# Kernel tuning notes

Hardware: AMD Instinct MI355X
Metric: run time of the kernel (lower is better)

Reference implementation:

```python
import jax, jax.numpy as jnp
import numpy as np

D_FEAT = 8192   # feature-space dimension d
T_RES = 2048    # number of reservoir feature vectors
P_PARAMS = 16   # n_modes * ansatz_layers
ORDER = 16      # agp_krylov_order (Krylov/Lanczos subspace size)
DTAU = 0.08     # cfg.ite_dtau
REG = 1e-4      # cfg.agp_reg
EPS = 1e-15


def setup_inputs() -> dict:
    key = jax.random.key(0)
    k1, k2, k3 = jax.random.split(key, 3)
    f = jax.random.normal(k1, (D_FEAT,), jnp.float32)
    # scale so spectral radius of H = -R^T R times DTAU is O(1)
    R = jax.random.normal(k2, (T_RES, D_FEAT), jnp.float32) * 0.02
    D = jax.random.normal(k3, (P_PARAMS, D_FEAT), jnp.float32)
    return {"f": f, "R": R, "D": D}


def _forward(f, R, D):
    d = f.shape[0]
    l = ORDER

    def apply_H(v):
        # H v = -sum_t f_t (f_t . v)  == -R^T (R v), matrix-free, memory-bound
        return -jnp.einsum('td,t->d', R, jnp.einsum('td,d->t', R, v))

    # ITE residual F = -(H - E) f, E = <f, Hf> / <f, f>
    Hf = apply_H(f)
    E = jnp.dot(f, Hf) / (jnp.dot(f, f) + EPS)
    F = -(Hf - E * f)
    normF = jnp.linalg.norm(F)

    # Lanczos with full reorthogonalisation; Q has l+1 rows (last is scratch)
    Q0 = jnp.zeros((l + 1, d), f.dtype).at[0].set(F / normF)
    alpha0 = jnp.zeros((l,), f.dtype)
    beta0 = jnp.zeros((l,), f.dtype)

    def step(carry, j):
        Q, alpha, beta = carry
        qj = Q[j]
        w = apply_H(qj)
        a = jnp.dot(qj, w)
        alpha = alpha.at[j].set(a)
        w = w - a * qj
        jm1 = jnp.maximum(j - 1, 0)
        bprev = jnp.where(j > 0, beta[jm1], jnp.array(0.0, f.dtype))
        w = w - bprev * Q[jm1]
        # full reorthogonalisation; rows > j of Q are zero so this projects
        # exactly onto span{q_0..q_j} like the original k-loop
        w = w - jnp.einsum('kd,k->d', Q, jnp.einsum('kd,d->k', Q, w))
        b = jnp.linalg.norm(w)
        beta = beta.at[j].set(b)
        Q = Q.at[j + 1].set(w / jnp.maximum(b, 1e-30))
        return (Q, alpha, beta), None

    (Q, alpha, beta), _ = jax.lax.scan(step, (Q0, alpha0, beta0), jnp.arange(l))
    Qb = Q[:l]          # (l, d) orthonormal Krylov basis
    off = beta[:l - 1]  # off-diagonal of tridiagonal T

    # Krylov exponential: exp(-H dtau) F ~= ||F|| * Q^T expm(-T dtau) e0
    Tmat = jnp.diag(alpha) + jnp.diag(off, 1) + jnp.diag(off, -1)
    evals, V = jnp.linalg.eigh(Tmat)
    coeffs = normF * (V @ (jnp.exp(-evals * DTAU) * V[0]))
    direction = jnp.einsum('l,ld->d', coeffs, Qb)

    # per-parameter diagonal projection: dtheta_i = <df_i, dir>/(||df_i||^2 + reg)
    dtheta = (D @ direction) / (jnp.sum(D * D, axis=1) + REG)
    return dtheta


def reference(f, R, D):
    return _forward(f, R, D)
```

## Files before the change

### kernel.cpp

```cpp
#include <hip/hip_runtime.h>
#include <math.h>

#define D_FEAT 8192
#define NC4    2048
#define T_RES  2048
#define LORD   16

#define NTHR 512
#define NBLK 256
#define RPT  32
#define NBAR 40
#define LPAD 16

#define G_COEF  0
#define G_BARC  16
#define G_RELW  (G_BARC + NBAR*64*LPAD)
#define G_ZEND  (G_RELW + NBAR*64*LPAD)
#define G_URAW  G_ZEND
#define G_UUP   (G_URAW + 17*2048)
#define G_FFP   (G_UUP + 256)
#define G_B2P   (G_FFP + 256)
#define G_DP    (G_B2P + 16*256)
#define G_NUMP  (G_DP + 16*17*256)
#define G_DENP  (G_NUMP + 16*256)
#define G_UPB   ((G_DENP + 16*256 + 1023) & ~1023)

__device__ __forceinline__ void astore(float* p, float v) {
    __hip_atomic_store(p, v, __ATOMIC_RELAXED, __HIP_MEMORY_SCOPE_AGENT);
}
__device__ __forceinline__ unsigned aloadu(const unsigned* p) {
    return __hip_atomic_load(p, __ATOMIC_RELAXED, __HIP_MEMORY_SCOPE_AGENT);
}

__device__ __forceinline__ void gbar(unsigned* cnt, unsigned* rel,
                                     int idx, int bid) {
    __syncthreads();
    const int tid = threadIdx.x;
    if (tid == 0)
        __hip_atomic_fetch_add(&cnt[(idx*64 + (bid & 63))*LPAD], 1u,
                               __ATOMIC_RELAXED, __HIP_MEMORY_SCOPE_AGENT);
    if (bid == 0) {
        if (tid < 64) {
            while (aloadu(&cnt[(idx*64 + tid)*LPAD]) < 4u)
                __builtin_amdgcn_s_sleep(1);
            __hip_atomic_store(&rel[(idx*64 + tid)*LPAD], 1u,
                               __ATOMIC_RELAXED, __HIP_MEMORY_SCOPE_AGENT);
        }
    } else if (tid == 0) {
        while (aloadu(&rel[(idx*64 + (bid & 63))*LPAD]) == 0u)
            __builtin_amdgcn_s_sleep(1);
    }
    __syncthreads();
}

__device__ __forceinline__ float wave_sum64(float s) {
    #pragma unroll
    for (int m = 1; m < 64; m <<= 1) s += __shfl_xor(s, m, 64);
    return s;
}

__device__ __forceinline__ void u_pass_lds(const float4 (&rr)[RPT],
                                           const float* wsl, float* ubuf,
                                           int rg, int cg) {
    const float4 w4 = ((const float4*)wsl)[cg];
    #pragma unroll
    for (int i = 0; i < RPT; ++i) {
        float d = rr[i].x*w4.x + rr[i].y*w4.y + rr[i].z*w4.z + rr[i].w*w4.w;
        d += __shfl_xor(d, 1, 64);
        d += __shfl_xor(d, 2, 64);
        d += __shfl_xor(d, 4, 64);
        if (cg == 0) ubuf[rg + 64*i] = d;
    }
}

__device__ __forceinline__ void flush_up(float* UP, const float* ubuf,
                                         int bid, int tid) {
    #pragma unroll
    for (int r = 0; r < 4; ++r) {
        const int t = tid + 512*r;
        astore(&UP[(size_t)(t >> 3)*2048 + bid*8 + (tid & 7)], ubuf[t]);
    }
}

__device__ __forceinline__ void reduce_up(const float* __restrict__ UP,
                                          float* udst, float (*red2)[8],
                                          float* ufin, float* uhrow,
                                          int bid, int tid) {
    const int off = tid & 7, g = tid >> 3;
    const float* base = UP + (size_t)bid*2048;
    float s = 0.f;
    #pragma unroll
    for (int i = 0; i < 4; ++i) s += base[(4*g + i)*8 + off];
    red2[g][off] = s;
    __syncthreads();
    if (tid < 8) {
        float u = 0.f;
        #pragma unroll
        for (int g2 = 0; g2 < 64; ++g2) u += red2[g2][tid];
        ufin[tid] = u;
        uhrow[tid] = u;
        astore(&udst[8*bid + tid], u);
    }
    __syncthreads();
}

__device__ __forceinline__ float4 y_pass(const float4 (&rr)[RPT],
                                         const float* u, int rg) {
    float4 acc = make_float4(0.f, 0.f, 0.f, 0.f);
    #pragma unroll
    for (int i = 0; i < RPT; ++i) {
        const float ut = u[rg + 64*i];
        acc.x -= ut*rr[i].x; acc.y -= ut*rr[i].y;
        acc.z -= ut*rr[i].z; acc.w -= ut*rr[i].w;
    }
    return acc;
}

__device__ __forceinline__ void y_reduce(float4 acc, float (*red)[8][4],
                                         float* ysl, int wave, int lane, int tid) {
    #pragma unroll
    for (int m = 8; m < 64; m <<= 1) {
        acc.x += __shfl_xor(acc.x, m, 64); acc.y += __shfl_xor(acc.y, m, 64);
        acc.z += __shfl_xor(acc.z, m, 64); acc.w += __shfl_xor(acc.w, m, 64);
    }
    if (lane < 8) {
        red[wave][lane][0] = acc.x; red[wave][lane][1] = acc.y;
        red[wave][lane][2] = acc.z; red[wave][lane][3] = acc.w;
    }
    __syncthreads();
    if (tid < 32) {
        const int g = tid >> 2, comp = tid & 3;
        float s = 0.f;
        #pragma unroll
        for (int w = 0; w < 8; ++w) s += red[w][g][comp];
        ysl[g*4 + comp] = s;
    }
    __syncthreads();
}

__global__ __launch_bounds__(NTHR, 2) void k_all(
    const float* __restrict__ Rm, const float* __restrict__ f,
    const float* __restrict__ Dm, float* __restrict__ out,
    float* __restrict__ ws)
{
    __shared__ __align__(16) float ubuf[2048];
    __shared__ float red2[64][8];
    __shared__ float red[8][8][4];
    __shared__ float ufin[8];
    __shared__ float uh[17][8];
    __shared__ __align__(16) float ysl[32];
    __shared__ __align__(16) float dirs[32];
    __shared__ __align__(16) float fsl[32];
    __shared__ float Wh[LORD][32];
    __shared__ float bh[LORD];
    __shared__ float alph[LORD];
    __shared__ float dotl[LORD];
    __shared__ float cf[LORD];
    __shared__ float misc[4];

    float* coefg   = ws + G_COEF;
    unsigned* barc = (unsigned*)(ws + G_BARC);
    unsigned* relw = (unsigned*)(ws + G_RELW);
    float* uraw = ws + G_URAW;
    float* UUP  = ws + G_UUP;
    float* FFP  = ws + G_FFP;
    float* B2P  = ws + G_B2P;
    float* DP   = ws + G_DP;
    float* NUMP = ws + G_NUMP;
    float* DENP = ws + G_DENP;
    float* UPB  = ws + G_UPB;
    int bar = 0;

    const int tid = threadIdx.x, bid = blockIdx.x;
    const int cg = tid & 7, rg = tid >> 3;
    const int lane = tid & 63, wave = tid >> 6;

    const float4* R4 = (const float4*)Rm;
    float4 rr[RPT];
    #pragma unroll
    for (int i = 0; i < RPT; ++i)
        rr[i] = R4[(size_t)(rg + 64*i)*NC4 + (bid << 3) + cg];

    if (wave == 0) {
        float4 fv = make_float4(0.f, 0.f, 0.f, 0.f);
        if (lane < 8) { fv = ((const float4*)f)[(bid << 3) + lane];
                        ((float4*)fsl)[lane] = fv; }
        float s2 = fv.x*fv.x + fv.y*fv.y + fv.z*fv.z + fv.w*fv.w;
        s2 += __shfl_xor(s2, 1, 64);
        s2 += __shfl_xor(s2, 2, 64);
        s2 += __shfl_xor(s2, 4, 64);
        if (lane == 0) astore(&FFP[bid], s2);
    }
    __syncthreads();
    u_pass_lds(rr, fsl, ubuf, rg, cg);
    __syncthreads();
    flush_up(UPB + (size_t)16*NBLK*2048, ubuf, bid, tid);
    gbar(barc, relw, bar++, bid);

    reduce_up(UPB + (size_t)16*NBLK*2048, uraw + 16*2048, red2, ufin, uh[16],
              bid, tid);
    if (tid == 0) {
        float pd = 0.f;
        #pragma unroll
        for (int t = 0; t < 8; ++t) pd += ufin[t]*ufin[t];
        astore(&UUP[bid], pd);
    }
    if (wave == 1) {
        float s = 0.f;
        #pragma unroll
        for (int i = 0; i < 4; ++i) s += FFP[lane + 64*i];
        s = wave_sum64(s);
        if (lane == 0) misc[2] = s;
    }
    gbar(barc, relw, bar++, bid);

    if (wave == 0) {
        float s = 0.f;
        #pragma unroll
        for (int i = 0; i < 4; ++i) s += UUP[lane + 64*i];
        s = wave_sum64(s);
        if (lane == 0) misc[3] = s;
    }
    #pragma unroll
    for (int r = 0; r < 4; ++r)
        ubuf[tid + 512*r] = uraw[16*2048 + tid + 512*r];
    __syncthreads();
    {
        float4 acc = y_pass(rr, ubuf, rg);
        y_reduce(acc, red, ysl, wave, lane, tid);
        const float E = -misc[3] / (misc[2] + 1e-15f);
        float v = 0.f;
        if (tid < 32) { v = E*fsl[tid] - ysl[tid]; Wh[0][tid] = v; }
        if (wave == 0) {
            float s = (lane < 32) ? v*v : 0.f;
            s = wave_sum64(s);
            if (lane == 0) astore(&B2P[0*256 + bid], s);
        }
        __syncthreads();
        u_pass_lds(rr, Wh[0], ubuf, rg, cg);
        __syncthreads();
        flush_up(UPB + (size_t)0*NBLK*2048, ubuf, bid, tid);
    }
    gbar(barc, relw, bar++, bid);

    for (int j = 0; j < LORD; ++j) {
        float* UPj = UPB + (size_t)j*NBLK*2048;
        float* DPj = DP + (size_t)j*17*256;
        reduce_up(UPj, uraw + (size_t)j*2048, red2, ufin, uh[j], bid, tid);
        if (wave == 0 && lane <= j) {
            float pd = 0.f;
            #pragma unroll 1
            for (int t = 0; t < 8; ++t) pd += ufin[t] * uh[lane][t];
            astore(&DPj[lane*256 + bid], pd);
        }
        if (wave == 1) {
            float s = 0.f;
            #pragma unroll
            for (int i = 0; i < 4; ++i) s += B2P[j*256 + lane + 64*i];
            s = wave_sum64(s);
            if (lane == 0) misc[0] = s;
        }
        gbar(barc, relw, bar++, bid);

        float tmp[4];
        if (j < LORD - 1) {
            #pragma unroll
            for (int r = 0; r < 4; ++r)
                tmp[r] = uraw[(size_t)j*2048 + tid + 512*r];
        }
        for (int k = wave; k <= j; k += 8) {
            float s = 0.f;
            #pragma unroll
            for (int i = 0; i < 4; ++i) s += DPj[k*256 + lane + 64*i];
            s = wave_sum64(s);
            if (lane == 0) dotl[k] = s;
        }
        __syncthreads();
        const float b2j = misc[0];
        const float bj  = sqrtf(fmaxf(b2j, 1e-60f));
        if (tid == 0) {
            bh[j]   = bj;
            alph[j] = -dotl[j] / fmaxf(b2j, 1e-60f);
        }
        if (j < LORD - 1) {
            const float inv = 1.0f / bj;
            #pragma unroll
            for (int r = 0; r < 4; ++r) ubuf[tid + 512*r] = tmp[r] * inv;
            __syncthreads();
            float4 acc = y_pass(rr, ubuf, rg);
            y_reduce(acc, red, ysl, wave, lane, tid);
            float v = 0.f;
            if (tid < 32) {
                v = ysl[tid];
                for (int k = 0; k <= j; ++k)
                    v += (dotl[k] / (bj * bh[k] * bh[k])) * Wh[k][tid];
                Wh[j+1][tid] = v;
            }
            if (wave == 0) {
                float s = (lane < 32) ? v*v : 0.f;
                s = wave_sum64(s);
                if (lane == 0) astore(&B2P[(j+1)*256 + bid], s);
            }
            __syncthreads();
            u_pass_lds(rr, Wh[j+1], ubuf, rg, cg);
            __syncthreads();
            flush_up(UPB + (size_t)(j+1)*NBLK*2048, ubuf, bid, tid);
        } else {
            __syncthreads();
            if (bid == 0 && wave == 0) {
                double a = 0.0, bl = 0.0;
                if (lane < LORD)     a  = (double)alph[lane];
                if (lane < LORD - 1) bl = (double)bh[lane + 1];
                double bprev = __shfl_up(bl, 1, 64);
                if (lane == 0) bprev = 0.0;
                if (lane >= LORD) { a = 0.0; bl = 0.0; bprev = 0.0; }
                double v = (lane == 0) ? 1.0 : 0.0;
                double accd = v;
                for (int n = 1; n <= 30; ++n) {
                    double vm = __shfl_up(v, 1, 64);
                    if (lane == 0) vm = 0.0;
                    double vp = __shfl_down(v, 1, 64);
                    if (lane >= LORD - 1) vp = 0.0;
                    const double tv = a*v + bprev*vm + bl*vp;
                    v = tv * (-0.08 / (double)n);
                    accd += v;
                }
                if (lane < LORD)
                    astore(&coefg[lane], (float)accd * bh[0]);
            }
        }
        gbar(barc, relw, bar++, bid);
    }

    if (wave == 0 && lane < 16) cf[lane] = coefg[lane];
    __syncthreads();
    if (tid < 32) {
        float s = 0.f;
        #pragma unroll
        for (int l = 0; l < LORD; ++l) s += cf[l] * Wh[l][tid] / bh[l];
        dirs[tid] = s;
    }
    __syncthreads();
    if (wave == 0 && lane < 16) {
        const float4* Dp = (const float4*)Dm + (size_t)lane*NC4 + (bid << 3);
        float num = 0.f, den = 0.f;
        #pragma unroll
        for (int g = 0; g < 8; ++g) {
            const float4 dv = Dp[g];
            const float4 dr = ((const float4*)dirs)[g];
            num += dv.x*dr.x + dv.y*dr.y + dv.z*dr.z + dv.w*dr.w;
            den += dv.x*dv.x + dv.y*dv.y + dv.z*dv.z + dv.w*dv.w;
        }
        astore(&NUMP[lane*256 + bid], num);
        astore(&DENP[lane*256 + bid], den);
    }
    gbar(barc, relw, bar++, bid);

    if (bid == 0) {
        for (int p = wave; p < 16; p += 8) {
            float n = 0.f, d = 0.f;
            #pragma unroll
            for (int i = 0; i < 4; ++i) {
                n += NUMP[p*256 + lane + 64*i];
                d += DENP[p*256 + lane + 64*i];
            }
            n = wave_sum64(n);
            d = wave_sum64(d);
            if (lane == 0) out[p] = n / (d + 1e-4f);
        }
    }
}

extern "C" void kernel_launch(void* const* d_in, const int* in_sizes, int n_in,
                              void* d_out, int out_size, void* d_ws, size_t ws_size,
                              hipStream_t stream)
{
    (void)in_sizes; (void)n_in; (void)out_size; (void)ws_size;
    const float* f  = (const float*)d_in[0];
    const float* Rm = (const float*)d_in[1];
    const float* Dm = (const float*)d_in[2];
    float* outp = (float*)d_out;
    float* ws   = (float*)d_ws;
    hipMemsetAsync(ws, 0, G_ZEND * sizeof(float), stream);
    void* args[] = { (void*)&Rm, (void*)&f, (void*)&Dm, (void*)&outp, (void*)&ws };
    hipLaunchCooperativeKernel((const void*)k_all, dim3(NBLK), dim3(NTHR),
                               args, 0, stream);
}
```

Baseline: 310.5 us.

## Replace centralized grid barrier with per-block flags and all-poll waits

Replaces the counter/release grid barrier, where block 0 gathers arrivals and then releases everyone, with per-block flag arrays. Each block sets its flag and 64 lanes poll all 256 flags directly, which removes the serial gather-then-release round trip. The partial u-pass results are now written straight to global memory instead of staging through LDS, and only block 0 waits at the final barrier. In exchange every block polls 256 flags at each barrier, adding memory traffic, and the flags depend on the workspace being zeroed before each launch.

New measurement: 383.7 us. +23.6%, slower.

```diff
diff --git a/kernel.cpp b/kernel.cpp
--- a/kernel.cpp
+++ b/kernel.cpp
@@ -9,13 +9,13 @@
 #define NTHR 512
 #define NBLK 256
 #define RPT  32
-#define NBAR 40
-#define LPAD 16
 
 #define G_COEF  0
-#define G_BARC  16
-#define G_RELW  (G_BARC + NBAR*64*LPAD)
-#define G_ZEND  (G_RELW + NBAR*64*LPAD)
+#define G_FUP   16
+#define G_FRED  (G_FUP + 17*256)
+#define G_FCOEF (G_FRED + 17*256)
+#define G_FNUM  (G_FCOEF + 16)
+#define G_ZEND  (G_FNUM + 256)
 #define G_URAW  G_ZEND
 #define G_UUP   (G_URAW + 17*2048)
 #define G_FFP   (G_UUP + 256)
@@ -28,27 +28,26 @@
 __device__ __forceinline__ void astore(float* p, float v) {
     __hip_atomic_store(p, v, __ATOMIC_RELAXED, __HIP_MEMORY_SCOPE_AGENT);
 }
+__device__ __forceinline__ void astoreu(unsigned* p, unsigned v) {
+    __hip_atomic_store(p, v, __ATOMIC_RELAXED, __HIP_MEMORY_SCOPE_AGENT);
+}
 __device__ __forceinline__ unsigned aloadu(const unsigned* p) {
     return __hip_atomic_load(p, __ATOMIC_RELAXED, __HIP_MEMORY_SCOPE_AGENT);
 }
 
-__device__ __forceinline__ void gbar(unsigned* cnt, unsigned* rel,
-                                     int idx, int bid) {
-    __syncthreads();
-    const int tid = threadIdx.x;
-    if (tid == 0)
-        __hip_atomic_fetch_add(&cnt[(idx*64 + (bid & 63))*LPAD], 1u,
-                               __ATOMIC_RELAXED, __HIP_MEMORY_SCOPE_AGENT);
-    if (bid == 0) {
-        if (tid < 64) {
-            while (aloadu(&cnt[(idx*64 + tid)*LPAD]) < 4u)
-                __builtin_amdgcn_s_sleep(1);
-            __hip_atomic_store(&rel[(idx*64 + tid)*LPAD], 1u,
-                               __ATOMIC_RELAXED, __HIP_MEMORY_SCOPE_AGENT);
-        }
-    } else if (tid == 0) {
-        while (aloadu(&rel[(idx*64 + (bid & 63))*LPAD]) == 0u)
+__device__ __forceinline__ void sigflag(unsigned* fl, int bid) {
+    __syncthreads();
+    if (threadIdx.x == 0) astoreu(&fl[bid], 1u);
+}
+
+__device__ __forceinline__ void pollall(const unsigned* fl) {
+    if (threadIdx.x < 64) {
+        const unsigned* p = fl + 4*threadIdx.x;
+        for (;;) {
+            unsigned a = aloadu(p) & aloadu(p+1) & aloadu(p+2) & aloadu(p+3);
+            if (__all((int)a)) break;
             __builtin_amdgcn_s_sleep(1);
+        }
     }
     __syncthreads();
 }
@@ -59,9 +58,9 @@
     return s;
 }
 
-__device__ __forceinline__ void u_pass_lds(const float4 (&rr)[RPT],
-                                           const float* wsl, float* ubuf,
-                                           int rg, int cg) {
+__device__ __forceinline__ void u_pass_store(const float4 (&rr)[RPT],
+                                             const float* wsl, float* UP,
+                                             int rg, int cg, int bid) {
     const float4 w4 = ((const float4*)wsl)[cg];
     #pragma unroll
     for (int i = 0; i < RPT; ++i) {
@@ -69,16 +68,10 @@
         d += __shfl_xor(d, 1, 64);
         d += __shfl_xor(d, 2, 64);
         d += __shfl_xor(d, 4, 64);
-        if (cg == 0) ubuf[rg + 64*i] = d;
-    }
-}
-
-__device__ __forceinline__ void flush_up(float* UP, const float* ubuf,
-                                         int bid, int tid) {
-    #pragma unroll
-    for (int r = 0; r < 4; ++r) {
-        const int t = tid + 512*r;
-        astore(&UP[(size_t)(t >> 3)*2048 + bid*8 + (tid & 7)], ubuf[t]);
+        if (cg == 0) {
+            const int t = rg + 64*i;
+            astore(&UP[(size_t)(t >> 3)*2048 + bid*8 + (t & 7)], d);
+        }
     }
 }
 
@@ -158,9 +151,11 @@
     __shared__ float cf[LORD];
     __shared__ float misc[4];
 
-    float* coefg   = ws + G_COEF;
-    unsigned* barc = (unsigned*)(ws + G_BARC);
-    unsigned* relw = (unsigned*)(ws + G_RELW);
+    float* coefg    = ws + G_COEF;
+    unsigned* fup   = (unsigned*)(ws + G_FUP);
+    unsigned* fred  = (unsigned*)(ws + G_FRED);
+    unsigned* fcoef = (unsigned*)(ws + G_FCOEF);
+    unsigned* fnum  = (unsigned*)(ws + G_FNUM);
     float* uraw = ws + G_URAW;
     float* UUP  = ws + G_UUP;
     float* FFP  = ws + G_FFP;
@@ -169,7 +164,6 @@
     float* NUMP = ws + G_NUMP;
     float* DENP = ws + G_DENP;
     float* UPB  = ws + G_UPB;
-    int bar = 0;
 
     const int tid = threadIdx.x, bid = blockIdx.x;
     const int cg = tid & 7, rg = tid >> 3;
@@ -192,10 +186,9 @@
         if (lane == 0) astore(&FFP[bid], s2);
     }
     __syncthreads();
-    u_pass_lds(rr, fsl, ubuf, rg, cg);
-    __syncthreads();
-    flush_up(UPB + (size_t)16*NBLK*2048, ubuf, bid, tid);
-    gbar(barc, relw, bar++, bid);
+    u_pass_store(rr, fsl, UPB + (size_t)16*NBLK*2048, rg, cg, bid);
+    sigflag(fup + 16*256, bid);
+    pollall(fup + 16*256);
 
     reduce_up(UPB + (size_t)16*NBLK*2048, uraw + 16*2048, red2, ufin, uh[16],
               bid, tid);
@@ -212,7 +205,8 @@
         s = wave_sum64(s);
         if (lane == 0) misc[2] = s;
     }
-    gbar(barc, relw, bar++, bid);
+    sigflag(fred + 16*256, bid);
+    pollall(fred + 16*256);
 
     if (wave == 0) {
         float s = 0.f;
@@ -237,11 +231,10 @@
             if (lane == 0) astore(&B2P[0*256 + bid], s);
         }
         __syncthreads();
-        u_pass_lds(rr, Wh[0], ubuf, rg, cg);
-        __syncthreads();
-        flush_up(UPB + (size_t)0*NBLK*2048, ubuf, bid, tid);
-    }
-    gbar(barc, relw, bar++, bid);
+        u_pass_store(rr, Wh[0], UPB + (size_t)0*NBLK*2048, rg, cg, bid);
+    }
+    sigflag(fup + 0*256, bid);
+    pollall(fup + 0*256);
 
     for (int j = 0; j < LORD; ++j) {
         float* UPj = UPB + (size_t)j*NBLK*2048;
@@ -260,7 +253,8 @@
             s = wave_sum64(s);
             if (lane == 0) misc[0] = s;
         }
-        gbar(barc, relw, bar++, bid);
+        sigflag(fred + j*256, bid);
+        pollall(fred + j*256);
 
         float tmp[4];
         if (j < LORD - 1) {
@@ -302,9 +296,9 @@
                 if (lane == 0) astore(&B2P[(j+1)*256 + bid], s);
             }
             __syncthreads();
-            u_pass_lds(rr, Wh[j+1], ubuf, rg, cg);
-            __syncthreads();
-            flush_up(UPB + (size_t)(j+1)*NBLK*2048, ubuf, bid, tid);
+            u_pass_store(rr, Wh[j+1], UPB + (size_t)(j+1)*NBLK*2048, rg, cg, bid);
+            sigflag(fup + (j+1)*256, bid);
+            pollall(fup + (j+1)*256);
         } else {
             __syncthreads();
             if (bid == 0 && wave == 0) {
@@ -328,8 +322,12 @@
                 if (lane < LORD)
                     astore(&coefg[lane], (float)accd * bh[0]);
             }
-        }
-        gbar(barc, relw, bar++, bid);
+            __syncthreads();
+            if (bid == 0 && tid == 0) astoreu(fcoef, 1u);
+            if (tid == 0)
+                while (aloadu(fcoef) == 0u) __builtin_amdgcn_s_sleep(1);
+            __syncthreads();
+        }
     }
 
     if (wave == 0 && lane < 16) cf[lane] = coefg[lane];
@@ -354,9 +352,10 @@
         astore(&NUMP[lane*256 + bid], num);
         astore(&DENP[lane*256 + bid], den);
     }
-    gbar(barc, relw, bar++, bid);
+    sigflag(fnum, bid);
 
     if (bid == 0) {
+        pollall(fnum);
         for (int p = wave; p < 16; p += 8) {
             float n = 0.f, d = 0.f;
             #pragma unroll
```

## Replace centralized grid barriers with flag-based split reduction by owner blocks

Applied to the files above, without the earlier changes.

Replaces the two-phase counter/release grid barrier with per-stage flag arrays, replicated for polling. The partial-sum reduction of R·v is now done by 32 owner blocks, each reducing 64 entries, while all blocks wait on a bitmask flag. It also makes the final gather wait only in block 0. The goal is to cut barrier latency and the number of full grid synchronisations in each Lanczos step. The cost is more complex synchronisation that depends on all blocks being co-resident and on flags being cleared between launches.

Measured after the change: 314.1 us. No clear change (+1.2%).

```diff
diff --git a/kernel.cpp b/kernel.cpp
--- a/kernel.cpp
+++ b/kernel.cpp
@@ -9,53 +9,74 @@
 #define NTHR 512
 #define NBLK 256
 #define RPT  32
-#define NBAR 40
-#define LPAD 16
+#define NOWN 32
+#define CH   64
+#define NREPA 4
+#define NREPB 16
 
 #define G_COEF  0
-#define G_BARC  16
-#define G_RELW  (G_BARC + NBAR*64*LPAD)
-#define G_ZEND  (G_RELW + NBAR*64*LPAD)
+#define G_FUPA  16
+#define G_FREDB (G_FUPA + 17*NREPA*256)
+#define G_FCOEF (G_FREDB + 17*NREPB*16)
+#define G_FNUM  (G_FCOEF + NREPB*16)
+#define G_ZEND  (G_FNUM + NREPA*256)
 #define G_URAW  G_ZEND
 #define G_UUP   (G_URAW + 17*2048)
-#define G_FFP   (G_UUP + 256)
+#define G_FFP   (G_UUP + 32)
 #define G_B2P   (G_FFP + 256)
 #define G_DP    (G_B2P + 16*256)
-#define G_NUMP  (G_DP + 16*17*256)
+#define G_NUMP  (G_DP + 16*16*32)
 #define G_DENP  (G_NUMP + 16*256)
 #define G_UPB   ((G_DENP + 16*256 + 1023) & ~1023)
+#define UPSLOT  (NOWN*NBLK*CH)
 
 __device__ __forceinline__ void astore(float* p, float v) {
     __hip_atomic_store(p, v, __ATOMIC_RELAXED, __HIP_MEMORY_SCOPE_AGENT);
 }
+__device__ __forceinline__ void astoreu(unsigned* p, unsigned v) {
+    __hip_atomic_store(p, v, __ATOMIC_RELAXED, __HIP_MEMORY_SCOPE_AGENT);
+}
 __device__ __forceinline__ unsigned aloadu(const unsigned* p) {
     return __hip_atomic_load(p, __ATOMIC_RELAXED, __HIP_MEMORY_SCOPE_AGENT);
 }
 
-__device__ __forceinline__ void gbar(unsigned* cnt, unsigned* rel,
-                                     int idx, int bid) {
-    __syncthreads();
-    const int tid = threadIdx.x;
-    if (tid == 0)
-        __hip_atomic_fetch_add(&cnt[(idx*64 + (bid & 63))*LPAD], 1u,
-                               __ATOMIC_RELAXED, __HIP_MEMORY_SCOPE_AGENT);
-    if (bid == 0) {
-        if (tid < 64) {
-            while (aloadu(&cnt[(idx*64 + tid)*LPAD]) < 4u)
-                __builtin_amdgcn_s_sleep(1);
-            __hip_atomic_store(&rel[(idx*64 + tid)*LPAD], 1u,
-                               __ATOMIC_RELAXED, __HIP_MEMORY_SCOPE_AGENT);
-        }
-    } else if (tid == 0) {
-        while (aloadu(&rel[(idx*64 + (bid & 63))*LPAD]) == 0u)
-            __builtin_amdgcn_s_sleep(1);
-    }
+__device__ __forceinline__ void sigA(unsigned* fl, int bid) {
+    __syncthreads();
+    if (threadIdx.x < NREPA) astoreu(&fl[threadIdx.x*256 + bid], 1u);
+}
+__device__ __forceinline__ void pollA(const unsigned* fl, int bid) {
+    if (threadIdx.x < 64) {
+        const unsigned* p = fl + (bid & (NREPA-1))*256 + 4*threadIdx.x;
+        for (;;) {
+            unsigned a = aloadu(p) & aloadu(p+1) & aloadu(p+2) & aloadu(p+3);
+            if (__all((int)a)) break;
+            __builtin_amdgcn_s_sleep(2);
+        }
+    }
+    __syncthreads();
+}
+
+__device__ __forceinline__ void sigB(unsigned* fl, int bid) {
+    __syncthreads();
+    if (threadIdx.x < NREPB)
+        __hip_atomic_fetch_or(&fl[threadIdx.x*16], 1u << bid,
+                              __ATOMIC_RELAXED, __HIP_MEMORY_SCOPE_AGENT);
+}
+__device__ __forceinline__ void pollB(const unsigned* fl, int bid) {
+    if (threadIdx.x == 0)
+        while (aloadu(&fl[(bid & (NREPB-1))*16]) != 0xFFFFFFFFu)
+            __builtin_amdgcn_s_sleep(2);
     __syncthreads();
 }
 
 __device__ __forceinline__ float wave_sum64(float s) {
     #pragma unroll
     for (int m = 1; m < 64; m <<= 1) s += __shfl_xor(s, m, 64);
+    return s;
+}
+__device__ __forceinline__ float sum32(float s) {
+    #pragma unroll
+    for (int m = 1; m < 32; m <<= 1) s += __shfl_xor(s, m, 64);
     return s;
 }
 
@@ -78,28 +99,28 @@
     #pragma unroll
     for (int r = 0; r < 4; ++r) {
         const int t = tid + 512*r;
-        astore(&UP[(size_t)(t >> 3)*2048 + bid*8 + (tid & 7)], ubuf[t]);
-    }
-}
-
-__device__ __forceinline__ void reduce_up(const float* __restrict__ UP,
-                                          float* udst, float (*red2)[8],
-                                          float* ufin, float* uhrow,
-                                          int bid, int tid) {
-    const int off = tid & 7, g = tid >> 3;
-    const float* base = UP + (size_t)bid*2048;
+        astore(&UP[(size_t)(t >> 6)*(NBLK*CH) + bid*CH + (t & 63)], ubuf[t]);
+    }
+}
+
+__device__ __forceinline__ void reduce_up64(const float* __restrict__ UP,
+                                            float* udst, float (*red8)[CH],
+                                            float* ufin64, float* uhrow,
+                                            int bid, int tid) {
+    const int r = tid & 63, bg = tid >> 6;
+    const float* base = UP + (size_t)bid*(NBLK*CH);
     float s = 0.f;
     #pragma unroll
-    for (int i = 0; i < 4; ++i) s += base[(4*g + i)*8 + off];
-    red2[g][off] = s;
-    __syncthreads();
-    if (tid < 8) {
+    for (int m = 0; m < 32; ++m) s += base[(bg*32 + m)*CH + r];
+    red8[bg][r] = s;
+    __syncthreads();
+    if (tid < 64) {
         float u = 0.f;
         #pragma unroll
-        for (int g2 = 0; g2 < 64; ++g2) u += red2[g2][tid];
-        ufin[tid] = u;
+        for (int g = 0; g < 8; ++g) u += red8[g][tid];
+        ufin64[tid] = u;
         uhrow[tid] = u;
-        astore(&udst[8*bid + tid], u);
+        astore(&udst[bid*CH + tid], u);
     }
     __syncthreads();
 }
@@ -144,10 +165,10 @@
     float* __restrict__ ws)
 {
     __shared__ __align__(16) float ubuf[2048];
-    __shared__ float red2[64][8];
+    __shared__ float red8[8][CH];
     __shared__ float red[8][8][4];
-    __shared__ float ufin[8];
-    __shared__ float uh[17][8];
+    __shared__ float ufin64[CH];
+    __shared__ float uh[17][CH];
     __shared__ __align__(16) float ysl[32];
     __shared__ __align__(16) float dirs[32];
     __shared__ __align__(16) float fsl[32];
@@ -158,9 +179,11 @@
     __shared__ float cf[LORD];
     __shared__ float misc[4];
 
-    float* coefg   = ws + G_COEF;
-    unsigned* barc = (unsigned*)(ws + G_BARC);
-    unsigned* relw = (unsigned*)(ws + G_RELW);
+    float* coefg    = ws + G_COEF;
+    unsigned* fupA  = (unsigned*)(ws + G_FUPA);
+    unsigned* fredB = (unsigned*)(ws + G_FREDB);
+    unsigned* fcoef = (unsigned*)(ws + G_FCOEF);
+    unsigned* fnum  = (unsigned*)(ws + G_FNUM);
     float* uraw = ws + G_URAW;
     float* UUP  = ws + G_UUP;
     float* FFP  = ws + G_FFP;
@@ -169,11 +192,11 @@
     float* NUMP = ws + G_NUMP;
     float* DENP = ws + G_DENP;
     float* UPB  = ws + G_UPB;
-    int bar = 0;
 
     const int tid = threadIdx.x, bid = blockIdx.x;
     const int cg = tid & 7, rg = tid >> 3;
     const int lane = tid & 63, wave = tid >> 6;
+    const bool owner = bid < NOWN;
 
     const float4* R4 = (const float4*)Rm;
     float4 rr[RPT];
@@ -194,16 +217,26 @@
     __syncthreads();
     u_pass_lds(rr, fsl, ubuf, rg, cg);
     __syncthreads();
-    flush_up(UPB + (size_t)16*NBLK*2048, ubuf, bid, tid);
-    gbar(barc, relw, bar++, bid);
-
-    reduce_up(UPB + (size_t)16*NBLK*2048, uraw + 16*2048, red2, ufin, uh[16],
-              bid, tid);
-    if (tid == 0) {
-        float pd = 0.f;
-        #pragma unroll
-        for (int t = 0; t < 8; ++t) pd += ufin[t]*ufin[t];
-        astore(&UUP[bid], pd);
+    flush_up(UPB + (size_t)16*UPSLOT, ubuf, bid, tid);
+    sigA(fupA + 16*NREPA*256, bid);
+
+    if (owner) {
+        pollA(fupA + 16*NREPA*256, bid);
+        reduce_up64(UPB + (size_t)16*UPSLOT, uraw + 16*2048, red8, ufin64,
+                    uh[16], bid, tid);
+        if (wave == 0) {
+            float p = ufin64[lane]*ufin64[lane];
+            p = wave_sum64(p);
+            if (lane == 0) astore(&UUP[bid], p);
+        }
+        sigB(fredB + 16*NREPB*16, bid);
+    }
+    pollB(fredB + 16*NREPB*16, bid);
+
+    if (wave == 0) {
+        float s = (lane < NOWN) ? UUP[lane] : 0.f;
+        s = sum32(s);
+        if (lane == 0) misc[3] = s;
     }
     if (wave == 1) {
         float s = 0.f;
@@ -211,15 +244,6 @@
         for (int i = 0; i < 4; ++i) s += FFP[lane + 64*i];
         s = wave_sum64(s);
         if (lane == 0) misc[2] = s;
-    }
-    gbar(barc, relw, bar++, bid);
-
-    if (wave == 0) {
-        float s = 0.f;
-        #pragma unroll
-        for (int i = 0; i < 4; ++i) s += UUP[lane + 64*i];
-        s = wave_sum64(s);
-        if (lane == 0) misc[3] = s;
     }
     #pragma unroll
     for (int r = 0; r < 4; ++r)
@@ -239,19 +263,36 @@
         __syncthreads();
         u_pass_lds(rr, Wh[0], ubuf, rg, cg);
         __syncthreads();
-        flush_up(UPB + (size_t)0*NBLK*2048, ubuf, bid, tid);
-    }
-    gbar(barc, relw, bar++, bid);
+        flush_up(UPB + (size_t)0*UPSLOT, ubuf, bid, tid);
+    }
+    sigA(fupA + 0*NREPA*256, bid);
 
     for (int j = 0; j < LORD; ++j) {
-        float* UPj = UPB + (size_t)j*NBLK*2048;
-        float* DPj = DP + (size_t)j*17*256;
-        reduce_up(UPj, uraw + (size_t)j*2048, red2, ufin, uh[j], bid, tid);
-        if (wave == 0 && lane <= j) {
-            float pd = 0.f;
-            #pragma unroll 1
-            for (int t = 0; t < 8; ++t) pd += ufin[t] * uh[lane][t];
-            astore(&DPj[lane*256 + bid], pd);
+        float* UPj = UPB + (size_t)j*UPSLOT;
+        float* DPj = DP + j*(16*NOWN);
+        if (owner) {
+            pollA(fupA + j*NREPA*256, bid);
+            reduce_up64(UPj, uraw + (size_t)j*2048, red8, ufin64, uh[j],
+                        bid, tid);
+            for (int k = wave; k <= j; k += 8) {
+                float p = ufin64[lane] * uh[k][lane];
+                p = wave_sum64(p);
+                if (lane == 0) astore(&DPj[k*NOWN + bid], p);
+            }
+            sigB(fredB + j*NREPB*16, bid);
+        }
+        pollB(fredB + j*NREPB*16, bid);
+
+        float tmp[4];
+        if (j < LORD - 1) {
+            #pragma unroll
+            for (int r = 0; r < 4; ++r)
+                tmp[r] = uraw[(size_t)j*2048 + tid + 512*r];
+        }
+        for (int k = wave; k <= j; k += 8) {
+            float s = (lane < NOWN) ? DPj[k*NOWN + lane] : 0.f;
+            s = sum32(s);
+            if (lane == 0) dotl[k] = s;
         }
         if (wave == 1) {
             float s = 0.f;
@@ -259,21 +300,6 @@
             for (int i = 0; i < 4; ++i) s += B2P[j*256 + lane + 64*i];
             s = wave_sum64(s);
             if (lane == 0) misc[0] = s;
-        }
-        gbar(barc, relw, bar++, bid);
-
-        float tmp[4];
-        if (j < LORD - 1) {
-            #pragma unroll
-            for (int r = 0; r < 4; ++r)
-                tmp[r] = uraw[(size_t)j*2048 + tid + 512*r];
-        }
-        for (int k = wave; k <= j; k += 8) {
-            float s = 0.f;
-            #pragma unroll
-            for (int i = 0; i < 4; ++i) s += DPj[k*256 + lane + 64*i];
-            s = wave_sum64(s);
-            if (lane == 0) dotl[k] = s;
         }
         __syncthreads();
         const float b2j = misc[0];
@@ -304,7 +330,8 @@
             __syncthreads();
             u_pass_lds(rr, Wh[j+1], ubuf, rg, cg);
             __syncthreads();
-            flush_up(UPB + (size_t)(j+1)*NBLK*2048, ubuf, bid, tid);
+            flush_up(UPB + (size_t)(j+1)*UPSLOT, ubuf, bid, tid);
+            sigA(fupA + (j+1)*NREPA*256, bid);
         } else {
             __syncthreads();
             if (bid == 0 && wave == 0) {
@@ -328,8 +355,13 @@
                 if (lane < LORD)
                     astore(&coefg[lane], (float)accd * bh[0]);
             }
-        }
-        gbar(barc, relw, bar++, bid);
+            __syncthreads();
+            if (bid == 0 && tid < NREPB) astoreu(&fcoef[tid*16], 1u);
+            if (tid == 0)
+                while (aloadu(&fcoef[(bid & (NREPB-1))*16]) == 0u)
+                    __builtin_amdgcn_s_sleep(2);
+            __syncthreads();
+        }
     }
 
     if (wave == 0 && lane < 16) cf[lane] = coefg[lane];
@@ -354,9 +386,10 @@
         astore(&NUMP[lane*256 + bid], num);
         astore(&DENP[lane*256 + bid], den);
     }
-    gbar(barc, relw, bar++, bid);
+    sigA(fnum, bid);
 
     if (bid == 0) {
+        pollA(fnum, 0);
         for (int p = wave; p < 16; p += 8) {
             float n = 0.f, d = 0.f;
             #pragma unroll
```
